# Performance work log

Hardware: AMD Instinct MI355X
Metric: run time of the kernel (lower is better)

## Reference

```python
import jax, jax.numpy as jnp
import numpy as np

B, DIN, E, H, V = 1024, 512, 512, 1024, 4096
MAX_LEN = 32  # max_len=33 with force_eos=True -> 32 decode steps


def setup_inputs() -> dict:
    key = jax.random.key(0)
    ks = jax.random.split(key, 12)
    def u(k, shape, fan_in):
        s = 1.0 / np.sqrt(fan_in)
        return jax.random.uniform(k, shape, jnp.float32, -s, s)
    return {
        "x": jax.random.normal(ks[0], (B, DIN), jnp.float32),
        "W_agent": u(ks[1], (DIN, H), DIN),
        "b_agent": u(ks[2], (H,), DIN),
        "sos_embedding": 0.01 * jax.random.normal(ks[3], (E,), jnp.float32),
        "emb": jax.random.normal(ks[4], (V, E), jnp.float32),
        "W_ih": u(ks[5], (E, H), H),
        "W_hh": u(ks[6], (H, H), H),
        "b_ih": u(ks[7], (H,), H),
        "b_hh": u(ks[8], (H,), H),
        "W_out": u(ks[9], (H, V), H),
        "b_out": u(ks[10], (V,), H),
    }


def reference(x, W_agent, b_agent, sos_embedding, emb, W_ih, W_hh, b_ih, b_hh, W_out, b_out):
    h0 = x @ W_agent + b_agent                      # agent(x): [B, H]
    inp0 = jnp.broadcast_to(sos_embedding, (x.shape[0], E))

    def step(carry, _):
        inp, h = carry
        h = jnp.tanh(inp @ W_ih + h @ W_hh + b_ih + b_hh)   # RNNCell
        logp = jax.nn.log_softmax(h @ W_out + b_out, axis=1)  # [B, V]
        tok = jnp.argmax(logp, axis=1)                      # eval-mode sample
        lp = jnp.take_along_axis(logp, tok[:, None], axis=1)[:, 0]
        ent = -jnp.sum(jnp.exp(logp) * logp, axis=1)
        return (emb[tok], h), (tok, lp, ent)

    (_, _), (seq, lps, ents) = jax.lax.scan(step, (inp0, h0), None, length=MAX_LEN)
    seq = seq.T        # [B, MAX_LEN]
    lps = lps.T
    ents = ents.T
    # force_eos: append zero column
    zf = jnp.zeros((seq.shape[0], 1), jnp.float32)
    sequence = jnp.concatenate([seq, zf.astype(seq.dtype)], axis=1)
    logits = jnp.concatenate([lps, zf], axis=1)
    entropy = jnp.concatenate([ents, zf], axis=1)
    return sequence, logits, entropy
```

## Files before the change

kernel.cpp:

```cpp
#include <hip/hip_runtime.h>
#include <math.h>

#define B_   1024
#define DIN  512
#define EMB  512
#define H_   1024
#define V_   4096
#define TSTEPS 32
#define LEN  33

typedef __attribute__((ext_vector_type(8))) short short8_t;
typedef __attribute__((ext_vector_type(4))) float f32x4;

#define AH_P  131072
#define AI_P  65536
#define B3_P  196608

__device__ inline unsigned short bf16_rne(float f) {
  unsigned u = __builtin_bit_cast(unsigned, f);
  u += 0x7FFFu + ((u >> 16) & 1u);
  return (unsigned short)(u >> 16);
}
__device__ inline float bf16_to_f(unsigned short h) {
  unsigned u = ((unsigned)h) << 16;
  return __builtin_bit_cast(float, u);
}
struct S3 { short a, b, c; };
__device__ inline S3 split3(float w) {
  unsigned short h0 = bf16_rne(w);  float r1 = w - bf16_to_f(h0);
  unsigned short h1 = bf16_rne(r1); float r2 = r1 - bf16_to_f(h1);
  S3 r; r.a = (short)h0; r.b = (short)h1; r.c = (short)bf16_rne(r2);
  return r;
}

#define T2MERGE(M1,I1,M2,I2, o1,oi1,o2,oi2)                              \
  if (o1 > M1 || (o1 == M1 && oi1 < I1)) {                               \
    float _n2; int _ni2;                                                 \
    if (M1 > o2 || (M1 == o2 && I1 < oi2)) { _n2 = M1; _ni2 = I1; }      \
    else { _n2 = o2; _ni2 = oi2; }                                       \
    M1 = o1; I1 = oi1; M2 = _n2; I2 = _ni2;                              \
  } else if (o1 > M2 || (o1 == M2 && oi1 < I2)) { M2 = o1; I2 = oi1; }

#define GBT 4
#define GKC 256
__global__ __launch_bounds__(256) void k_gemm(
    float* __restrict__ out,
    const float* __restrict__ A1, int K1, const float* __restrict__ W1,
    const float* __restrict__ A2, int K2, const float* __restrict__ W2,
    const float* __restrict__ b1, const float* __restrict__ b2,
    int do_tanh)
{
  const int N = H_;
  __shared__ float sA[GBT][GKC];
  const int tid = threadIdx.x;
  const int bid = blockIdx.x;
  const int colb = (bid & 7) >> 1;
  const int rowb = ((bid >> 3) << 1) | (bid & 1);
  const int rb  = rowb * GBT;
  const int col = colb * 256 + tid;

  float acc[GBT];
  float bias = b1[col] + (b2 ? b2[col] : 0.0f);
#pragma unroll
  for (int r = 0; r < GBT; ++r) acc[r] = bias;

  const int nch = (K1 + K2) / GKC;
  for (int c = 0; c < nch; ++c) {
    const int kb = c * GKC;
    const float* A; const float* W; int k0, strideA;
    if (kb < K1) { A = A1; W = W1; k0 = kb;      strideA = K1; }
    else         { A = A2; W = W2; k0 = kb - K1; strideA = K2; }
    __syncthreads();
    {
      int r = tid >> 6, kk = (tid & 63) << 2;
      *(float4*)&sA[r][kk] = *(const float4*)(A + (size_t)(rb + r) * strideA + k0 + kk);
    }
    __syncthreads();
    const float* Wp = W + (size_t)k0 * N + col;
#pragma unroll 4
    for (int k = 0; k < GKC; k += 4) {
      float4 a0 = *(const float4*)&sA[0][k];
      float4 a1 = *(const float4*)&sA[1][k];
      float4 a2 = *(const float4*)&sA[2][k];
      float4 a3 = *(const float4*)&sA[3][k];
      float w0 = Wp[(size_t)k * N];
      float w1 = Wp[(size_t)(k + 1) * N];
      float w2 = Wp[(size_t)(k + 2) * N];
      float w3 = Wp[(size_t)(k + 3) * N];
      acc[0] = fmaf(a0.x, w0, acc[0]); acc[1] = fmaf(a1.x, w0, acc[1]);
      acc[2] = fmaf(a2.x, w0, acc[2]); acc[3] = fmaf(a3.x, w0, acc[3]);
      acc[0] = fmaf(a0.y, w1, acc[0]); acc[1] = fmaf(a1.y, w1, acc[1]);
      acc[2] = fmaf(a2.y, w1, acc[2]); acc[3] = fmaf(a3.y, w1, acc[3]);
      acc[0] = fmaf(a0.z, w2, acc[0]); acc[1] = fmaf(a1.z, w2, acc[1]);
      acc[2] = fmaf(a2.z, w2, acc[2]); acc[3] = fmaf(a3.z, w2, acc[3]);
      acc[0] = fmaf(a0.w, w3, acc[0]); acc[1] = fmaf(a1.w, w3, acc[1]);
      acc[2] = fmaf(a2.w, w3, acc[2]); acc[3] = fmaf(a3.w, w3, acc[3]);
    }
  }
#pragma unroll
  for (int r = 0; r < GBT; ++r) {
    float v = acc[r];
    if (do_tanh) v = tanhf(v);
    out[(size_t)(rb + r) * N + col] = v;
  }
}

__global__ __launch_bounds__(256) void k_prepack(
    const float* __restrict__ W, unsigned short* __restrict__ Bp)
{
  int t = blockIdx.x * 256 + threadIdx.x;
  int lane = t & 63;
  int ntg  = (t >> 6) & 255;
  int ks   = t >> 14;
  int col  = ntg * 16 + (lane & 15);
  int krow = ks * 32 + ((lane >> 4) << 3);
  short8_t hv;
#pragma unroll
  for (int j = 0; j < 8; ++j) {
    float w = W[(size_t)(krow + j) * V_ + col];
    hv[j] = (short)bf16_rne(w);
  }
  size_t base = ((size_t)ks * 256 + ntg) * 64 + lane;
  ((short8_t*)Bp)[base] = hv;
}

__global__ __launch_bounds__(256) void k_packW3(
    const float* __restrict__ Wih, const float* __restrict__ Whh,
    unsigned short* __restrict__ BU)
{
  int t = blockIdx.x * 256 + threadIdx.x;
  int lane = t & 63;
  int ntg  = (t >> 6) & 63;
  int ks   = t >> 12;
  int col  = ntg * 16 + (lane & 15);
  int krow = ks * 32 + ((lane >> 4) << 3);
  short8_t p0, p1, p2;
#pragma unroll
  for (int j = 0; j < 8; ++j) {
    int kr = krow + j;
    float w = (kr < DIN) ? Wih[(size_t)kr * H_ + col]
                         : Whh[(size_t)(kr - DIN) * H_ + col];
    S3 s = split3(w);
    p0[j] = s.a; p1[j] = s.b; p2[j] = s.c;
  }
  short8_t* o = (short8_t*)BU;
  size_t base = ((size_t)ks * 64 + ntg) * 64 + lane;
  o[base] = p0; o[base + B3_P] = p1; o[base + 2 * B3_P] = p2;
}

__global__ __launch_bounds__(256) void k_wtrans(
    const float* __restrict__ W, float* __restrict__ WT)
{
  __shared__ float tile[64][65];
  int kb = (blockIdx.x & 15) * 64;
  int vb = (blockIdx.x >> 4) * 64;
  int t = threadIdx.x;
  {
    int vv = t & 63, k0 = (t >> 6) * 16;
    for (int j = 0; j < 16; ++j)
      tile[k0 + j][vv] = W[(size_t)(kb + k0 + j) * V_ + vb + vv];
  }
  __syncthreads();
  {
    int kk = t & 63, v0 = (t >> 6) * 16;
    for (int j = 0; j < 16; ++j)
      WT[(size_t)(vb + v0 + j) * H_ + kb + kk] = tile[kk][v0 + j];
  }
}

__global__ __launch_bounds__(256) void k_packh(
    const float* __restrict__ h, unsigned short* __restrict__ AU)
{
  int t = blockIdx.x * 256 + threadIdx.x;
  int r = t >> 7, q = t & 127;
  int ks = q >> 2, kg = q & 3;
  int lanep = (r & 15) + (kg << 4);
  int rt = r >> 4;
  const float* src = h + (size_t)r * H_ + q * 8;
  float4 f0 = *(const float4*)src;
  float4 f1 = *(const float4*)(src + 4);
  float f[8] = {f0.x, f0.y, f0.z, f0.w, f1.x, f1.y, f1.z, f1.w};
  short8_t p0, p1, p2;
#pragma unroll
  for (int j = 0; j < 8; ++j) {
    S3 s = split3(f[j]);
    p0[j] = s.a; p1[j] = s.b; p2[j] = s.c;
  }
  short8_t* o = (short8_t*)AU;
  size_t base = (size_t)rt * 2048 + (size_t)ks * 64 + lanep;
  o[base] = p0; o[base + AH_P] = p1; o[base + 2 * AH_P] = p2;
}

__global__ __launch_bounds__(256) void k_sos3(
    const float* __restrict__ sos, unsigned short* __restrict__ AU)
{
  int wid = threadIdx.x >> 6, lane = threadIdx.x & 63;
  int row = blockIdx.x * 4 + wid;
  const float* src = sos + lane * 8;
  float4 f0 = *(const float4*)src;
  float4 f1 = *(const float4*)(src + 4);
  float f[8] = {f0.x, f0.y, f0.z, f0.w, f1.x, f1.y, f1.z, f1.w};
  short8_t p0, p1, p2;
#pragma unroll
  for (int j = 0; j < 8; ++j) {
    S3 s = split3(f[j]);
    p0[j] = s.a; p1[j] = s.b; p2[j] = s.c;
  }
  int ks = lane >> 2, kg = lane & 3;
  int lanep = (row & 15) + (kg << 4);
  int rt = row >> 4;
  short8_t* o = (short8_t*)AU;
  size_t base = (size_t)rt * 1024 + (size_t)ks * 64 + lanep;
  o[base] = p0; o[base + AI_P] = p1; o[base + 2 * AI_P] = p2;
}

__global__ __launch_bounds__(512) void k_rnn(
    const unsigned short* __restrict__ AinpU, const unsigned short* __restrict__ AhU,
    const unsigned short* __restrict__ Bw3U,
    const float* __restrict__ b1, const float* __restrict__ b2,
    float* __restrict__ hout, unsigned short* __restrict__ AhOutU)
{
  __shared__ float sh[64][65];
  const short8_t* Ainp = (const short8_t*)AinpU;
  const short8_t* Ah   = (const short8_t*)AhU;
  const short8_t* Bw3  = (const short8_t*)Bw3U;

  const int bid  = blockIdx.x;
  const int colb = ((bid & 7) << 1) | ((bid >> 3) & 1);
  const int rowb = bid >> 4;
  const int tid  = threadIdx.x, lane = tid & 63, wid = tid >> 6;
  const int wm = (wid >> 1) & 1, wn = wid & 1, kh = wid >> 2;
  const int l15 = lane & 15, lg = lane >> 4;

  f32x4 acc[2][2];
#pragma unroll
  for (int rt = 0; rt < 2; ++rt)
#pragma unroll
    for (int nt = 0; nt < 2; ++nt) {
      int col = colb * 64 + wn * 32 + nt * 16 + l15;
      float b = (kh == 0) ? (b1[col] + b2[col]) : 0.0f;
      acc[rt][nt] = (f32x4){b, b, b, b};
    }

  const int rt0 = rowb * 4 + wm * 2;
  const int ng0 = colb * 4 + wn * 2;
  const int ks0 = kh * 24;

#define RNN_LOAD(A_, B_, KS)                                                   \
  {                                                                            \
    int _ks = (KS);                                                            \
    if (_ks < 16) {                                                            \
      _Pragma("unroll") for (int rt = 0; rt < 2; ++rt)                         \
        _Pragma("unroll") for (int p = 0; p < 3; ++p)                          \
          A_[rt][p] = Ainp[(size_t)p * AI_P + (size_t)(rt0 + rt) * 1024 +      \
                           (size_t)_ks * 64 + lane];                           \
    } else {                                                                   \
      int _h = _ks - 16;                                                       \
      _Pragma("unroll") for (int rt = 0; rt < 2; ++rt)                         \
        _Pragma("unroll") for (int p = 0; p < 3; ++p)                          \
          A_[rt][p] = Ah[(size_t)p * AH_P + (size_t)(rt0 + rt) * 2048 +        \
                         (size_t)_h * 64 + lane];                              \
    }                                                                          \
    _Pragma("unroll") for (int nt = 0; nt < 2; ++nt)                           \
      _Pragma("unroll") for (int p = 0; p < 3; ++p)                            \
        B_[nt][p] = Bw3[(size_t)p * B3_P + (size_t)_ks * 4096 +                \
                        (size_t)(ng0 + nt) * 64 + lane];                       \
  }

  short8_t a[2][3], bb[2][3];
  RNN_LOAD(a, bb, ks0)
#pragma unroll
  for (int i = 0; i < 24; ++i) {
    short8_t an[2][3], bn[2][3];
    if (i < 23) RNN_LOAD(an, bn, ks0 + i + 1)
#pragma unroll
    for (int rt = 0; rt < 2; ++rt)
#pragma unroll
      for (int nt = 0; nt < 2; ++nt) {
        acc[rt][nt] = __builtin_amdgcn_mfma_f32_16x16x32_bf16(a[rt][0], bb[nt][0], acc[rt][nt], 0, 0, 0);
        acc[rt][nt] = __builtin_amdgcn_mfma_f32_16x16x32_bf16(a[rt][0], bb[nt][1], acc[rt][nt], 0, 0, 0);
        acc[rt][nt] = __builtin_amdgcn_mfma_f32_16x16x32_bf16(a[rt][1], bb[nt][0], acc[rt][nt], 0, 0, 0);
        acc[rt][nt] = __builtin_amdgcn_mfma_f32_16x16x32_bf16(a[rt][1], bb[nt][1], acc[rt][nt], 0, 0, 0);
        acc[rt][nt] = __builtin_amdgcn_mfma_f32_16x16x32_bf16(a[rt][0], bb[nt][2], acc[rt][nt], 0, 0, 0);
        acc[rt][nt] = __builtin_amdgcn_mfma_f32_16x16x32_bf16(a[rt][2], bb[nt][0], acc[rt][nt], 0, 0, 0);
      }
    if (i < 23) {
#pragma unroll
      for (int rt = 0; rt < 2; ++rt)
#pragma unroll
        for (int p = 0; p < 3; ++p) { a[rt][p] = an[rt][p]; bb[rt][p] = bn[rt][p]; }
    }
  }
#undef RNN_LOAD

  if (kh == 1) {
#pragma unroll
    for (int rt = 0; rt < 2; ++rt)
#pragma unroll
      for (int nt = 0; nt < 2; ++nt)
#pragma unroll
        for (int r = 0; r < 4; ++r)
          sh[wm * 32 + rt * 16 + lg * 4 + r][wn * 32 + nt * 16 + l15] = acc[rt][nt][r];
  }
  __syncthreads();
  if (kh == 0) {
#pragma unroll
    for (int rt = 0; rt < 2; ++rt)
#pragma unroll
      for (int nt = 0; nt < 2; ++nt)
#pragma unroll
        for (int r = 0; r < 4; ++r) {
          int lr = wm * 32 + rt * 16 + lg * 4 + r;
          int lc = wn * 32 + nt * 16 + l15;
          float v = tanhf(acc[rt][nt][r] + sh[lr][lc]);
          hout[(size_t)(rowb * 64 + lr) * H_ + colb * 64 + lc] = v;
          sh[lr][lc] = v;
        }
  }
  __syncthreads();
  {
    int lr = tid >> 3, q = tid & 7;
    int gk = colb * 64 + q * 8;
    int ks = gk >> 5, kg = (gk >> 3) & 3;
    int gr = rowb * 64 + lr;
    int lanep = (gr & 15) + (kg << 4);
    int rt = gr >> 4;
    short8_t p0, p1, p2;
#pragma unroll
    for (int j = 0; j < 8; ++j) {
      S3 s = split3(sh[lr][q * 8 + j]);
      p0[j] = s.a; p1[j] = s.b; p2[j] = s.c;
    }
    short8_t* o = (short8_t*)AhOutU;
    size_t base = (size_t)rt * 2048 + (size_t)ks * 64 + lanep;
    o[base] = p0; o[base + AH_P] = p1; o[base + 2 * AH_P] = p2;
  }
}

__global__ __launch_bounds__(256) void k_logits3(
    const unsigned short* __restrict__ AhU, const unsigned short* __restrict__ BpU,
    const float* __restrict__ bout, float4* __restrict__ partA,
    float4* __restrict__ partB)
{
  __shared__ float sred[2][2][32][6];
  __shared__ float sbmax[64];
  const short8_t* Ah = (const short8_t*)AhU;
  const short8_t* Bp = (const short8_t*)BpU;

  const int bid  = blockIdx.x;
  const int colb = ((bid & 7) << 2) | ((bid >> 3) & 3);
  const int rowb = bid >> 5;
  const int tid  = threadIdx.x, lane = tid & 63, wid = tid >> 6;
  const int wm = wid >> 1, wn = wid & 1;
  const int l15 = lane & 15, lg = lane >> 4;

  const int colbase = colb * 128 + wn * 64;
  f32x4 acc[2][4];
#pragma unroll
  for (int nt = 0; nt < 4; ++nt) {
    float b = bout[colbase + nt * 16 + l15];
    acc[0][nt] = (f32x4){b, b, b, b};
    acc[1][nt] = acc[0][nt];
  }
  const int rt0 = rowb * 4 + wm * 2;
  const int ng0 = colb * 8 + wn * 4;

#define LG_LOAD(A_, B_, KS)                                                    \
  {                                                                            \
    int _ks = (KS);                                                            \
    _Pragma("unroll") for (int rt = 0; rt < 2; ++rt)                           \
      A_[rt] = Ah[(size_t)(rt0 + rt) * 2048 + (size_t)_ks * 64 + lane];        \
    _Pragma("unroll") for (int nt = 0; nt < 4; ++nt)                           \
      B_[nt] = Bp[((size_t)_ks * 256 + ng0 + nt) * 64 + lane];                 \
  }

  short8_t abuf[3][2], bbuf[3][4];
  LG_LOAD(abuf[0], bbuf[0], 0)
  LG_LOAD(abuf[1], bbuf[1], 1)
#pragma unroll
  for (int ks = 0; ks < 32; ++ks) {
    const int cur = ks % 3, nxt = (ks + 2) % 3;
    if (ks + 2 < 32) LG_LOAD(abuf[nxt], bbuf[nxt], ks + 2)
#pragma unroll
    for (int rt = 0; rt < 2; ++rt)
#pragma unroll
      for (int nt = 0; nt < 4; ++nt)
        acc[rt][nt] = __builtin_amdgcn_mfma_f32_16x16x32_bf16(
            abuf[cur][rt], bbuf[cur][nt], acc[rt][nt], 0, 0, 0);
  }
#undef LG_LOAD

#pragma unroll
  for (int rt = 0; rt < 2; ++rt)
#pragma unroll
    for (int r = 0; r < 4; ++r) {
      float M1 = -1e30f, M2 = -1e30f; int I1 = 0, I2 = 0;
#pragma unroll
      for (int nt = 0; nt < 4; ++nt) {
        float v = acc[rt][nt][r]; int c = colbase + nt * 16 + l15;
        if (v > M1) { M2 = M1; I2 = I1; M1 = v; I1 = c; }
        else if (v > M2) { M2 = v; I2 = c; }
      }
#pragma unroll
      for (int d = 1; d < 16; d <<= 1) {
        float o1 = __shfl_xor(M1, d); int oi1 = __shfl_xor(I1, d);
        float o2 = __shfl_xor(M2, d); int oi2 = __shfl_xor(I2, d);
        T2MERGE(M1, I1, M2, I2, o1, oi1, o2, oi2)
      }
      if (l15 == 0) {
        int rl = rt * 16 + lg * 4 + r;
        sred[wm][wn][rl][0] = M1; sred[wm][wn][rl][1] = (float)I1;
        sred[wm][wn][rl][2] = M2; sred[wm][wn][rl][3] = (float)I2;
      }
    }
  __syncthreads();
  if (tid < 64) {
    int wmm = tid >> 5, rl = tid & 31;
    float M1 = sred[wmm][0][rl][0]; int I1 = (int)sred[wmm][0][rl][1];
    float M2 = sred[wmm][0][rl][2]; int I2 = (int)sred[wmm][0][rl][3];
    float o1 = sred[wmm][1][rl][0]; int oi1 = (int)sred[wmm][1][rl][1];
    float o2 = sred[wmm][1][rl][2]; int oi2 = (int)sred[wmm][1][rl][3];
    T2MERGE(M1, I1, M2, I2, o1, oi1, o2, oi2)
    int row = rowb * 64 + wmm * 32 + rl;
    partA[(size_t)row * 32 + colb] = make_float4(M1, (float)I1, M2, (float)I2);
    sbmax[wmm * 32 + rl] = M1;
  }
  __syncthreads();
#pragma unroll
  for (int rt = 0; rt < 2; ++rt)
#pragma unroll
    for (int r = 0; r < 4; ++r) {
      float m = sbmax[wm * 32 + rt * 16 + lg * 4 + r];
      float s = 0.f, tsum = 0.f;
#pragma unroll
      for (int nt = 0; nt < 4; ++nt) {
        float d = acc[rt][nt][r] - m;
        float e = expf(d);
        s += e; tsum += d * e;
      }
#pragma unroll
      for (int d = 1; d < 16; d <<= 1) { s += __shfl_xor(s, d); tsum += __shfl_xor(tsum, d); }
      if (l15 == 0) {
        int rl = rt * 16 + lg * 4 + r;
        sred[wm][wn][rl][4] = s; sred[wm][wn][rl][5] = tsum;
      }
    }
  __syncthreads();
  if (tid < 64) {
    int wmm = tid >> 5, rl = tid & 31;
    float s = sred[wmm][0][rl][4] + sred[wmm][1][rl][4];
    float tsum = sred[wmm][0][rl][5] + sred[wmm][1][rl][5];
    int row = rowb * 64 + wmm * 32 + rl;
    partB[(size_t)row * 32 + colb] = make_float4(s, tsum, 0.f, 0.f);
  }
}

__global__ __launch_bounds__(256) void k_finalize3(
    const float4* __restrict__ partA, const float4* __restrict__ partB,
    const float* __restrict__ h, const float* __restrict__ Wout,
    const float* __restrict__ WoutT, const float* __restrict__ bout,
    const float* __restrict__ emb, float* __restrict__ out,
    unsigned short* __restrict__ AinpU, int tstep)
{
  const int lane = threadIdx.x & 63;
  const int wid  = threadIdx.x >> 6;
  const int row  = blockIdx.x * 4 + wid;

  float M1 = -1e30f, M2 = -1e30f; int I1 = 0, I2 = 0;
  float bm = -1e30f, s_l = 0.f, t_l = 0.f;
  if (lane < 32) {
    float4 pa = partA[(size_t)row * 32 + lane];
    float4 pb = partB[(size_t)row * 32 + lane];
    M1 = pa.x; I1 = (int)pa.y; M2 = pa.z; I2 = (int)pa.w;
    bm = pa.x; s_l = pb.x; t_l = pb.y;
  }
  for (int d = 1; d < 32; d <<= 1) {
    float o1 = __shfl_xor(M1, d); int oi1 = __shfl_xor(I1, d);
    float o2 = __shfl_xor(M2, d); int oi2 = __shfl_xor(I2, d);
    T2MERGE(M1, I1, M2, I2, o1, oi1, o2, oi2)
  }
  M1 = __shfl(M1, 0); I1 = __shfl(I1, 0);
  M2 = __shfl(M2, 0); I2 = __shfl(I2, 0);

  float e = (lane < 32) ? expf(bm - M1) : 0.f;
  float s = e * s_l;
  float tsum = e * (t_l + (bm - M1) * s_l);
  for (int d = 1; d < 64; d <<= 1) { s += __shfl_xor(s, d); tsum += __shfl_xor(tsum, d); }

  const float* hrow = h + (size_t)row * H_;
  float d1 = 0.f, d2 = 0.f;
  if (WoutT) {
    const float* w1 = WoutT + (size_t)I1 * H_;
    const float* w2 = WoutT + (size_t)I2 * H_;
#pragma unroll 4
    for (int k = lane; k < H_; k += 64) {
      float hv = hrow[k];
      d1 = fmaf(hv, w1[k], d1);
      d2 = fmaf(hv, w2[k], d2);
    }
  } else {
    for (int k = lane; k < H_; k += 64) {
      float hv = hrow[k];
      d1 = fmaf(hv, Wout[(size_t)k * V_ + I1], d1);
      d2 = fmaf(hv, Wout[(size_t)k * V_ + I2], d2);
    }
  }
  for (int d = 1; d < 64; d <<= 1) { d1 += __shfl_xor(d1, d); d2 += __shfl_xor(d2, d); }
  d1 += bout[I1]; d2 += bout[I2];

  int tok; float ltok;
  if (d2 > d1 || (d2 == d1 && I2 < I1)) { tok = I2; ltok = d2; }
  else                                  { tok = I1; ltok = d1; }
  float lg_s = logf(s);
  if (lane == 0) {
    out[(size_t)row * LEN + tstep]                  = (float)tok;
    out[(size_t)(B_ * LEN) + row * LEN + tstep]     = ltok - M1 - lg_s;
    out[(size_t)(2 * B_ * LEN) + row * LEN + tstep] = lg_s - tsum / s;
  }
  const float* er = emb + (size_t)tok * EMB + lane * 8;
  float4 f0 = *(const float4*)er;
  float4 f1 = *(const float4*)(er + 4);
  float f[8] = {f0.x, f0.y, f0.z, f0.w, f1.x, f1.y, f1.z, f1.w};
  short8_t p0, p1, p2;
#pragma unroll
  for (int j = 0; j < 8; ++j) {
    S3 s3v = split3(f[j]);
    p0[j] = s3v.a; p1[j] = s3v.b; p2[j] = s3v.c;
  }
  int ks = lane >> 2, kg = lane & 3;
  int lanep = (row & 15) + (kg << 4);
  int rt = row >> 4;
  short8_t* o = (short8_t*)AinpU;
  size_t base = (size_t)rt * 1024 + (size_t)ks * 64 + lanep;
  o[base] = p0; o[base + AI_P] = p1; o[base + 2 * AI_P] = p2;
}

#define BT 16
#define KC 128
__global__ __launch_bounds__(256) void k_logits_f32(
    const float* __restrict__ h, const float* __restrict__ Wout,
    const float* __restrict__ bout, float4* __restrict__ part)
{
  __shared__ float sA[BT][KC];
  __shared__ float redf[4][BT];
  __shared__ float redf2[4][BT];
  __shared__ int   redi[4][BT];
  __shared__ float bm[BT];

  const int tid = threadIdx.x;
  const int rb  = blockIdx.x * BT;
  const int c0  = blockIdx.y * 512 + tid * 2;

  float acc[BT][2];
  float2 bj = *(const float2*)(bout + c0);
#pragma unroll
  for (int r = 0; r < BT; ++r) { acc[r][0] = bj.x; acc[r][1] = bj.y; }

  for (int kb = 0; kb < H_; kb += KC) {
    __syncthreads();
    {
      float4* s4 = (float4*)sA;
#pragma unroll
      for (int i = 0; i < 2; ++i) {
        int idx = tid + i * 256;
        int r = idx >> 5, kk = (idx & 31) << 2;
        s4[idx] = *(const float4*)(h + (size_t)(rb + r) * H_ + kb + kk);
      }
    }
    __syncthreads();
    const float* Wp = Wout + (size_t)kb * V_ + c0;
#pragma unroll 2
    for (int k = 0; k < KC; k += 4) {
      float4 a[BT];
#pragma unroll
      for (int r = 0; r < BT; ++r) a[r] = *((const float4*)sA[r] + (k >> 2));
      float2 w[4];
#pragma unroll
      for (int u = 0; u < 4; ++u) w[u] = *(const float2*)(Wp + (size_t)(k + u) * V_);
#pragma unroll
      for (int u = 0; u < 4; ++u)
#pragma unroll
        for (int r = 0; r < BT; ++r) {
          float av = ((const float*)&a[r])[u];
          acc[r][0] = fmaf(av, w[u].x, acc[r][0]);
          acc[r][1] = fmaf(av, w[u].y, acc[r][1]);
        }
    }
  }

  const int wid = tid >> 6, lane = tid & 63;
  float mx[BT]; int ix[BT];
#pragma unroll
  for (int r = 0; r < BT; ++r) {
    float m = acc[r][0]; int ii = c0;
    if (acc[r][1] > m) { m = acc[r][1]; ii = c0 + 1; }
    mx[r] = m; ix[r] = ii;
  }
#pragma unroll
  for (int r = 0; r < BT; ++r) {
    for (int d = 32; d; d >>= 1) {
      float ov = __shfl_xor(mx[r], d);
      int   oi = __shfl_xor(ix[r], d);
      if (ov > mx[r] || (ov == mx[r] && oi < ix[r])) { mx[r] = ov; ix[r] = oi; }
    }
  }
  if (lane == 0) {
#pragma unroll
    for (int r = 0; r < BT; ++r) { redf[wid][r] = mx[r]; redi[wid][r] = ix[r]; }
  }
  __syncthreads();
  if (tid < BT) {
    float m = redf[0][tid]; int ii = redi[0][tid];
    for (int w = 1; w < 4; ++w) {
      float ov = redf[w][tid]; int oi = redi[w][tid];
      if (ov > m || (ov == m && oi < ii)) { m = ov; ii = oi; }
    }
    bm[tid] = m; redi[0][tid] = ii;
  }
  __syncthreads();
  float ss[BT], tt[BT];
#pragma unroll
  for (int r = 0; r < BT; ++r) {
    float m = bm[r];
    float s = 0.f, t = 0.f;
#pragma unroll
    for (int j = 0; j < 2; ++j) {
      float d = acc[r][j] - m;
      float e2 = expf(d);
      s += e2; t += d * e2;
    }
    ss[r] = s; tt[r] = t;
  }
#pragma unroll
  for (int r = 0; r < BT; ++r) {
    for (int d = 32; d; d >>= 1) {
      ss[r] += __shfl_xor(ss[r], d);
      tt[r] += __shfl_xor(tt[r], d);
    }
  }
  if (lane == 0) {
#pragma unroll
    for (int r = 0; r < BT; ++r) { redf[wid][r] = ss[r]; redf2[wid][r] = tt[r]; }
  }
  __syncthreads();
  if (tid < BT) {
    float s = 0.f, t = 0.f;
    for (int w = 0; w < 4; ++w) { s += redf[w][tid]; t += redf2[w][tid]; }
    part[(size_t)(rb + tid) * 8 + blockIdx.y] =
        make_float4(bm[tid], s, t, (float)redi[0][tid]);
  }
}

__global__ __launch_bounds__(128) void k_finalize_f32(
    const float4* __restrict__ part, const float* __restrict__ emb,
    float* __restrict__ out, float* __restrict__ inp, int t)
{
  const int row = blockIdx.x;
  __shared__ int s_tok;
  if (threadIdx.x == 0) {
    float4 p[8];
#pragma unroll
    for (int i = 0; i < 8; ++i) p[i] = part[(size_t)row * 8 + i];
    float m = p[0].x; int tok = (int)p[0].w;
#pragma unroll
    for (int i = 1; i < 8; ++i)
      if (p[i].x > m) { m = p[i].x; tok = (int)p[i].w; }
    float S = 0.f, T = 0.f;
#pragma unroll
    for (int i = 0; i < 8; ++i) {
      float w = expf(p[i].x - m);
      S += w * p[i].y;
      T += w * (p[i].z + (p[i].x - m) * p[i].y);
    }
    float lp  = -logf(S);
    float ent = logf(S) - T / S;
    out[(size_t)row * LEN + t]                  = (float)tok;
    out[(size_t)(B_ * LEN) + row * LEN + t]     = lp;
    out[(size_t)(2 * B_ * LEN) + row * LEN + t] = ent;
    s_tok = tok;
  }
  __syncthreads();
  const float4* src = (const float4*)(emb + (size_t)s_tok * EMB);
  float4* dst = (float4*)(inp + (size_t)row * EMB);
  for (int i = threadIdx.x; i < EMB / 4; i += blockDim.x) dst[i] = src[i];
}

__global__ void k_sos(const float* __restrict__ sos, float* __restrict__ inp) {
  int i = blockIdx.x * blockDim.x + threadIdx.x;
  ((float4*)inp)[i] = ((const float4*)sos)[i & (EMB / 4 - 1)];
}
__global__ void k_zero(float* __restrict__ out) {
  int i = blockIdx.x * blockDim.x + threadIdx.x;
  if (i < 3 * B_) {
    int sec = i >> 10, row = i & (B_ - 1);
    out[(size_t)sec * (B_ * LEN) + (size_t)row * LEN + (LEN - 1)] = 0.f;
  }
}

extern "C" void kernel_launch(void* const* d_in, const int* in_sizes, int n_in,
                              void* d_out, int out_size, void* d_ws, size_t ws_size,
                              hipStream_t stream) {
  const float* x       = (const float*)d_in[0];
  const float* W_agent = (const float*)d_in[1];
  const float* b_agent = (const float*)d_in[2];
  const float* sos     = (const float*)d_in[3];
  const float* emb     = (const float*)d_in[4];
  const float* W_ih    = (const float*)d_in[5];
  const float* W_hh    = (const float*)d_in[6];
  const float* b_ih    = (const float*)d_in[7];
  const float* b_hh    = (const float*)d_in[8];
  const float* W_out   = (const float*)d_in[9];
  const float* b_out   = (const float*)d_in[10];
  float* out = (float*)d_out;

  const size_t SZ_BPOUT = 8388608;
  const size_t SZ_BW3   = 9437184;
  const size_t SZ_WT    = 16777216;
  const size_t SZ_AH    = 6291456;
  const size_t SZ_AINP  = 3145728;
  const size_t SZ_H     = 4194304;
  const size_t SZ_PART  = 524288;
  const size_t NEED_A = SZ_BPOUT + SZ_BW3 + SZ_WT + 2 * SZ_AH + SZ_AINP + SZ_H + 2 * SZ_PART;
  const size_t NEED_B = NEED_A - SZ_WT;

  if (ws_size >= NEED_B) {
    const bool useT = ws_size >= NEED_A;
    char* p = (char*)d_ws;
    unsigned short* BpOut = (unsigned short*)p; p += SZ_BPOUT;
    unsigned short* Bw3   = (unsigned short*)p; p += SZ_BW3;
    float* WoutT = nullptr;
    if (useT) { WoutT = (float*)p; p += SZ_WT; }
    unsigned short* Ah0  = (unsigned short*)p; p += SZ_AH;
    unsigned short* Ah1  = (unsigned short*)p; p += SZ_AH;
    unsigned short* Ainp = (unsigned short*)p; p += SZ_AINP;
    float*  hbuf  = (float*)p; p += SZ_H;
    float4* partA = (float4*)p; p += SZ_PART;
    float4* partB = (float4*)p;

    k_sos3<<<dim3(256), dim3(256), 0, stream>>>(sos, Ainp);
    k_prepack<<<dim3(2048), dim3(256), 0, stream>>>(W_out, BpOut);
    k_packW3<<<dim3(768), dim3(256), 0, stream>>>(W_ih, W_hh, Bw3);
    if (useT) k_wtrans<<<dim3(1024), dim3(256), 0, stream>>>(W_out, WoutT);
    k_gemm<<<dim3(1024), dim3(256), 0, stream>>>(
        hbuf, x, DIN, W_agent, nullptr, 0, nullptr, b_agent, nullptr, 0);
    k_packh<<<dim3(512), dim3(256), 0, stream>>>(hbuf, Ah0);

    for (int t = 0; t < TSTEPS; ++t) {
      unsigned short* AhIn  = (t & 1) ? Ah1 : Ah0;
      unsigned short* AhOut = (t & 1) ? Ah0 : Ah1;
      k_rnn<<<dim3(256), dim3(512), 0, stream>>>(
          Ainp, AhIn, Bw3, b_ih, b_hh, hbuf, AhOut);
      k_logits3<<<dim3(512), dim3(256), 0, stream>>>(
          AhOut, BpOut, b_out, partA, partB);
      k_finalize3<<<dim3(256), dim3(256), 0, stream>>>(
          partA, partB, hbuf, W_out, WoutT, b_out, emb, out, Ainp, t);
    }
  } else {
    float*  h0buf = (float*)d_ws;
    float*  h1buf = h0buf + (size_t)B_ * H_;
    float*  inp   = h1buf + (size_t)B_ * H_;
    float4* part  = (float4*)(inp + (size_t)B_ * EMB);

    k_sos<<<dim3(B_ * EMB / 4 / 256), dim3(256), 0, stream>>>(sos, inp);
    k_gemm<<<dim3(1024), dim3(256), 0, stream>>>(
        h0buf, x, DIN, W_agent, nullptr, 0, nullptr, b_agent, nullptr, 0);
    for (int t = 0; t < TSTEPS; ++t) {
      float* hr = (t & 1) ? h1buf : h0buf;
      float* hw = (t & 1) ? h0buf : h1buf;
      k_gemm<<<dim3(1024), dim3(256), 0, stream>>>(
          hw, inp, EMB, W_ih, hr, H_, W_hh, b_ih, b_hh, 1);
      k_logits_f32<<<dim3(B_ / BT, V_ / 512), dim3(256), 0, stream>>>(
          hw, W_out, b_out, part);
      k_finalize_f32<<<dim3(B_), dim3(128), 0, stream>>>(part, emb, out, inp, t);
    }
  }
  k_zero<<<dim3(12), dim3(256), 0, stream>>>(out);
}
```

Baseline: 1.943 ms.

## Stage logits MFMA fragments in LDS via direct global-to-LDS loads

```diff
diff --git a/kernel.cpp b/kernel.cpp
--- a/kernel.cpp
+++ b/kernel.cpp
@@ -31,6 +31,12 @@
   unsigned short h1 = bf16_rne(r1); float r2 = r1 - bf16_to_f(h1);
   S3 r; r.a = (short)h0; r.b = (short)h1; r.c = (short)bf16_rne(r2);
   return r;
+}
+
+__device__ inline void load_lds16(const void* g, void* l) {
+  __builtin_amdgcn_global_load_lds(
+      (__attribute__((address_space(1))) void*)g,
+      (__attribute__((address_space(3))) void*)l, 16, 0, 0);
 }
 
 #define T2MERGE(M1,I1,M2,I2, o1,oi1,o2,oi2)                              \
@@ -337,11 +343,12 @@
   }
 }
 
-__global__ __launch_bounds__(256) void k_logits3(
+__global__ __launch_bounds__(256) void k_logits5(
     const unsigned short* __restrict__ AhU, const unsigned short* __restrict__ BpU,
     const float* __restrict__ bout, float4* __restrict__ partA,
     float4* __restrict__ partB)
 {
+  __shared__ short8_t frag[2][12][64];
   __shared__ float sred[2][2][32][6];
   __shared__ float sbmax[64];
   const short8_t* Ah = (const short8_t*)AhU;
@@ -354,7 +361,10 @@
   const int wm = wid >> 1, wn = wid & 1;
   const int l15 = lane & 15, lg = lane >> 4;
 
+  const int rt0 = rowb * 4;
+  const int ng0 = colb * 8;
   const int colbase = colb * 128 + wn * 64;
+
   f32x4 acc[2][4];
 #pragma unroll
   for (int nt = 0; nt < 4; ++nt) {
@@ -362,33 +372,41 @@
     acc[0][nt] = (f32x4){b, b, b, b};
     acc[1][nt] = acc[0][nt];
   }
-  const int rt0 = rowb * 4 + wm * 2;
-  const int ng0 = colb * 8 + wn * 4;
-
-#define LG_LOAD(A_, B_, KS)                                                    \
+
+#define STAGE(KS, BUF)                                                         \
   {                                                                            \
     int _ks = (KS);                                                            \
-    _Pragma("unroll") for (int rt = 0; rt < 2; ++rt)                           \
-      A_[rt] = Ah[(size_t)(rt0 + rt) * 2048 + (size_t)_ks * 64 + lane];        \
-    _Pragma("unroll") for (int nt = 0; nt < 4; ++nt)                           \
-      B_[nt] = Bp[((size_t)_ks * 256 + ng0 + nt) * 64 + lane];                 \
-  }
-
-  short8_t abuf[3][2], bbuf[3][4];
-  LG_LOAD(abuf[0], bbuf[0], 0)
-  LG_LOAD(abuf[1], bbuf[1], 1)
-#pragma unroll
+    _Pragma("unroll") for (int q = 0; q < 3; ++q) {                            \
+      int s = wid * 3 + q;                                                     \
+      const short8_t* g = (s < 4)                                              \
+          ? &Ah[(size_t)(rt0 + s) * 2048 + (size_t)_ks * 64 + lane]            \
+          : &Bp[((size_t)_ks * 256 + ng0 + (s - 4)) * 64 + lane];              \
+      load_lds16(g, &frag[BUF][s][0]);                                         \
+    }                                                                          \
+  }
+
+  STAGE(0, 0)
+  int cur = 0;
   for (int ks = 0; ks < 32; ++ks) {
-    const int cur = ks % 3, nxt = (ks + 2) % 3;
-    if (ks + 2 < 32) LG_LOAD(abuf[nxt], bbuf[nxt], ks + 2)
-#pragma unroll
-    for (int rt = 0; rt < 2; ++rt)
-#pragma unroll
-      for (int nt = 0; nt < 4; ++nt)
-        acc[rt][nt] = __builtin_amdgcn_mfma_f32_16x16x32_bf16(
-            abuf[cur][rt], bbuf[cur][nt], acc[rt][nt], 0, 0, 0);
-  }
-#undef LG_LOAD
+    __syncthreads();
+    if (ks < 31) STAGE(ks + 1, cur ^ 1)
+    short8_t a0 = frag[cur][wm * 2 + 0][lane];
+    short8_t a1 = frag[cur][wm * 2 + 1][lane];
+    short8_t b0 = frag[cur][4 + wn * 4 + 0][lane];
+    short8_t b1 = frag[cur][4 + wn * 4 + 1][lane];
+    short8_t b2 = frag[cur][4 + wn * 4 + 2][lane];
+    short8_t b3 = frag[cur][4 + wn * 4 + 3][lane];
+    acc[0][0] = __builtin_amdgcn_mfma_f32_16x16x32_bf16(a0, b0, acc[0][0], 0, 0, 0);
+    acc[0][1] = __builtin_amdgcn_mfma_f32_16x16x32_bf16(a0, b1, acc[0][1], 0, 0, 0);
+    acc[0][2] = __builtin_amdgcn_mfma_f32_16x16x32_bf16(a0, b2, acc[0][2], 0, 0, 0);
+    acc[0][3] = __builtin_amdgcn_mfma_f32_16x16x32_bf16(a0, b3, acc[0][3], 0, 0, 0);
+    acc[1][0] = __builtin_amdgcn_mfma_f32_16x16x32_bf16(a1, b0, acc[1][0], 0, 0, 0);
+    acc[1][1] = __builtin_amdgcn_mfma_f32_16x16x32_bf16(a1, b1, acc[1][1], 0, 0, 0);
+    acc[1][2] = __builtin_amdgcn_mfma_f32_16x16x32_bf16(a1, b2, acc[1][2], 0, 0, 0);
+    acc[1][3] = __builtin_amdgcn_mfma_f32_16x16x32_bf16(a1, b3, acc[1][3], 0, 0, 0);
+    cur ^= 1;
+  }
+#undef STAGE
 
 #pragma unroll
   for (int rt = 0; rt < 2; ++rt)
@@ -750,7 +768,7 @@
       unsigned short* AhOut = (t & 1) ? Ah0 : Ah1;
       k_rnn<<<dim3(256), dim3(512), 0, stream>>>(
           Ainp, AhIn, Bw3, b_ih, b_hh, hbuf, AhOut);
-      k_logits3<<<dim3(512), dim3(256), 0, stream>>>(
+      k_logits5<<<dim3(512), dim3(256), 0, stream>>>(
           AhOut, BpOut, b_out, partA, partB);
       k_finalize3<<<dim3(256), dim3(256), 0, stream>>>(
           partA, partB, hbuf, W_out, WoutT, b_out, emb, out, Ainp, t);
```

After: 2.153 ms. 1.11x slower.
